# Kernel tuning notes

Measured on AMD Instinct MI355X. Metric: run time of the kernel, lower is better.

The kernel has to match this reference:

```python
import jax, jax.numpy as jnp
import numpy as np

N_NODES = 50000
N_EDGES = 800000
ND = 64   # node_dim
HD = 128  # hidden_dim
ED = 32   # edge_dim


def setup_inputs() -> dict:
    key = jax.random.key(0)
    ks = jax.random.split(key, 16)
    init = lambda k, shape: (jax.random.normal(k, shape, jnp.float32)
                             / np.float32(np.sqrt(shape[0])))
    h = jax.random.normal(ks[0], (N_NODES, ND), jnp.float32)
    x = jax.random.normal(ks[1], (N_NODES, 3), jnp.float32) * 10.0
    edge_index = jax.random.randint(ks[2], (2, N_EDGES), 0, N_NODES, dtype=jnp.int64)
    # realistic edge distances = actual pairwise distances of sampled edges
    edge_dist = jnp.linalg.norm(x[edge_index[0]] - x[edge_index[1]], axis=-1)
    in_dim = 2 * ND + ED
    return {
        "h": h, "x": x, "edge_index": edge_index, "edge_dist": edge_dist,
        # edge_mlp: Linear(1, ED) -> SiLU -> Linear(ED, ED)
        "We1": init(ks[3], (1, ED)), "be1": jnp.zeros((ED,), jnp.float32),
        "We2": init(ks[4], (ED, ED)), "be2": jnp.zeros((ED,), jnp.float32),
        # node_mlp: Linear(in_dim, HD) -> SiLU -> Linear(HD, ND)
        "Wn1": init(ks[5], (in_dim, HD)), "bn1": jnp.zeros((HD,), jnp.float32),
        "Wn2": init(ks[6], (HD, ND)), "bn2": jnp.zeros((ND,), jnp.float32),
        # coord_mlp: Linear(in_dim, HD) -> SiLU -> Linear(HD, 1, bias=False)
        "Wc1": init(ks[7], (in_dim, HD)), "bc1": jnp.zeros((HD,), jnp.float32),
        "Wc2": init(ks[8], (HD, 1)),
    }


def reference(h, x, edge_index, edge_dist,
              We1, be1, We2, be2,
              Wn1, bn1, Wn2, bn2,
              Wc1, bc1, Wc2):
    n = h.shape[0]
    src, dst = edge_index[0], edge_index[1]
    # edge_mlp on scalar distance -> [E, ED]
    e = jax.nn.silu(edge_dist[:, None] @ We1 + be1) @ We2 + be2
    # gather + concat -> [E, 2*ND + ED]
    m_input = jnp.concatenate([h[src], h[dst], e], axis=-1)
    # node messages [E, ND]
    m = jax.nn.silu(m_input @ Wn1 + bn1) @ Wn2 + bn2
    h_agg = jax.ops.segment_sum(m, dst, num_segments=n)
    # coord update weight [E, 1]
    coord_weight = jax.nn.silu(m_input @ Wc1 + bc1) @ Wc2
    dir_vec = x[src] - x[dst]
    dir_len = jnp.clip(jnp.linalg.norm(dir_vec, axis=-1, keepdims=True), 1e-8)
    coord_update = coord_weight * (dir_vec / dir_len)
    x_agg = jax.ops.segment_sum(coord_update, dst, num_segments=n)
    return h + h_agg, x + x_agg
```

## Files before the change

kernel.cpp:

```cpp
#include <hip/hip_runtime.h>


#define NN 50000
#define NE 800000
#define NDIM 64
#define HDIM 128
#define EDIM 32
#define NTILES (NE / 64)
#define MSTRIDE 168
#define HSTRIDE 136
#define NH (NN * NDIM)
#define NX (NN * 3)

typedef __bf16 bf16x8 __attribute__((ext_vector_type(8)));
typedef float f32x4 __attribute__((ext_vector_type(4)));
typedef unsigned short ushort8 __attribute__((ext_vector_type(8)));
typedef unsigned short ushort4v __attribute__((ext_vector_type(4)));

__device__ __forceinline__ unsigned short f2bf(float f) {
    union { float f; unsigned int u; } c; c.f = f;
    unsigned int r = c.u + 0x7fffu + ((c.u >> 16) & 1u);
    return (unsigned short)(r >> 16);
}
__device__ __forceinline__ float bf2f(unsigned short u) {
    union { unsigned int u; float f; } c; c.u = ((unsigned int)u) << 16;
    return c.f;
}
__device__ __forceinline__ float silu(float v) { return v / (1.0f + __expf(-v)); }

__device__ __forceinline__ bf16x8 ld_frag(const unsigned short* p) {
    union { ushort8 u; bf16x8 v; } c;
    c.u = *(const ushort8*)p;
    return c.v;
}
__device__ __forceinline__ bf16x8 mk_frag(const unsigned short* u) {
    union { ushort8 uu; bf16x8 v; } c;
#pragma unroll
    for (int j = 0; j < 8; ++j) c.uu[j] = u[j];
    return c.v;
}

__global__ void init_out(const float* __restrict__ h, const float* __restrict__ x,
                         float* __restrict__ out) {
    int i = blockIdx.x * 256 + threadIdx.x;
    if (i < NH) out[i] = h[i];
    else if (i < NH + NX) out[i] = x[i - NH];
}

__global__ __launch_bounds__(256, 2) void egnn_edges(
    const float* __restrict__ h, const float* __restrict__ x,
    const int* __restrict__ srcg, const int* __restrict__ dstg,
    const float* __restrict__ dist,
    const float* __restrict__ We1, const float* __restrict__ be1,
    const float* __restrict__ We2, const float* __restrict__ be2,
    const float* __restrict__ Wn1, const float* __restrict__ bn1,
    const float* __restrict__ Wn2, const float* __restrict__ bn2,
    const float* __restrict__ Wc1, const float* __restrict__ bc1,
    const float* __restrict__ Wc2,
    float* __restrict__ outh, float* __restrict__ outx) {

    __shared__ __align__(16) unsigned short mlds[64 * MSTRIDE];
    __shared__ __align__(16) unsigned short hl[64 * HSTRIDE];
    __shared__ int src_l[64];
    __shared__ int dst_l[64];
    __shared__ float dist_l[64];
    __shared__ float we1_l[32], be1_l[32], be2_l[32];
    __shared__ float we2_l[32 * 32];
    __shared__ float wc2_l[128];
    __shared__ float part_l[256];

    const int tid  = threadIdx.x;
    const int w    = tid >> 6;
    const int lane = tid & 63;
    const int l15  = lane & 15;
    const int quad = lane >> 4;

    if (tid < 32) { we1_l[tid] = We1[tid]; be1_l[tid] = be1[tid]; be2_l[tid] = be2[tid]; }
    if (tid < 128) wc2_l[tid] = Wc2[tid];
    for (int i = tid; i < 1024; i += 256) we2_l[i] = We2[i];

    bf16x8 wn1f[5][2], wc1f[5][2];
#pragma unroll
    for (int kc = 0; kc < 5; ++kc) {
#pragma unroll
        for (int nt = 0; nt < 2; ++nt) {
            unsigned short un[8], uc[8];
            const int n = w * 32 + nt * 16 + l15;
#pragma unroll
            for (int j = 0; j < 8; ++j) {
                const int k = kc * 32 + quad * 8 + j;
                un[j] = f2bf(Wn1[k * HDIM + n]);
                uc[j] = f2bf(Wc1[k * HDIM + n]);
            }
            wn1f[kc][nt] = mk_frag(un);
            wc1f[kc][nt] = mk_frag(uc);
        }
    }
    bf16x8 wn2f[4];
#pragma unroll
    for (int kc = 0; kc < 4; ++kc) {
        unsigned short u[8];
        const int n = w * 16 + l15;
#pragma unroll
        for (int j = 0; j < 8; ++j) {
            const int k = kc * 32 + quad * 8 + j;
            u[j] = f2bf(Wn2[k * NDIM + n]);
        }
        wn2f[kc] = mk_frag(u);
    }
    const float biasN0 = bn1[w * 32 + l15];
    const float biasN1 = bn1[w * 32 + 16 + l15];
    const float biasC0 = bc1[w * 32 + l15];
    const float biasC1 = bc1[w * 32 + 16 + l15];
    const float bias2v = bn2[w * 16 + l15];

    for (int tile = blockIdx.x; tile < NTILES; tile += gridDim.x) {
        __syncthreads();

        if (tid < 64) {
            const int e = tile * 64 + tid;
            src_l[tid] = srcg[e];
            dst_l[tid] = dstg[e];
            dist_l[tid] = dist[e];
        }
        __syncthreads();

        {
            const int c4 = tid & 15, sub = tid >> 4;
#pragma unroll
            for (int it = 0; it < 4; ++it) {
                const int el = sub + it * 16;
                const float4 hs = *(const float4*)(h + (size_t)src_l[el] * NDIM + c4 * 4);
                const float4 hd = *(const float4*)(h + (size_t)dst_l[el] * NDIM + c4 * 4);
                ushort4v us = { f2bf(hs.x), f2bf(hs.y), f2bf(hs.z), f2bf(hs.w) };
                ushort4v ud = { f2bf(hd.x), f2bf(hd.y), f2bf(hd.z), f2bf(hd.w) };
                *(ushort4v*)&mlds[el * MSTRIDE + c4 * 4] = us;
                *(ushort4v*)&mlds[el * MSTRIDE + 64 + c4 * 4] = ud;
            }
        }
        {
            const int el = tid >> 2, part = tid & 3;
            const float dv = dist_l[el];
            float o[8];
#pragma unroll
            for (int j = 0; j < 8; ++j) o[j] = be2_l[part * 8 + j];
#pragma unroll
            for (int k = 0; k < 32; ++k) {
                const float sk = silu(dv * we1_l[k] + be1_l[k]);
#pragma unroll
                for (int j = 0; j < 8; ++j) o[j] += sk * we2_l[k * 32 + part * 8 + j];
            }
            ushort4v a = { f2bf(o[0]), f2bf(o[1]), f2bf(o[2]), f2bf(o[3]) };
            ushort4v b = { f2bf(o[4]), f2bf(o[5]), f2bf(o[6]), f2bf(o[7]) };
            *(ushort4v*)&mlds[el * MSTRIDE + 128 + part * 8] = a;
            *(ushort4v*)&mlds[el * MSTRIDE + 128 + part * 8 + 4] = b;
        }
        __syncthreads();

        f32x4 accN[4][2], accC[4][2];
#pragma unroll
        for (int mt = 0; mt < 4; ++mt) {
            accN[mt][0] = (f32x4){biasN0, biasN0, biasN0, biasN0};
            accN[mt][1] = (f32x4){biasN1, biasN1, biasN1, biasN1};
            accC[mt][0] = (f32x4){biasC0, biasC0, biasC0, biasC0};
            accC[mt][1] = (f32x4){biasC1, biasC1, biasC1, biasC1};
        }
#pragma unroll
        for (int kc = 0; kc < 5; ++kc) {
            bf16x8 af[4];
#pragma unroll
            for (int mt = 0; mt < 4; ++mt)
                af[mt] = ld_frag(&mlds[(mt * 16 + l15) * MSTRIDE + kc * 32 + quad * 8]);
#pragma unroll
            for (int mt = 0; mt < 4; ++mt) {
#pragma unroll
                for (int nt = 0; nt < 2; ++nt) {
                    accN[mt][nt] = __builtin_amdgcn_mfma_f32_16x16x32_bf16(
                        af[mt], wn1f[kc][nt], accN[mt][nt], 0, 0, 0);
                    accC[mt][nt] = __builtin_amdgcn_mfma_f32_16x16x32_bf16(
                        af[mt], wc1f[kc][nt], accC[mt][nt], 0, 0, 0);
                }
            }
        }

#pragma unroll
        for (int mt = 0; mt < 4; ++mt)
#pragma unroll
            for (int nt = 0; nt < 2; ++nt)
#pragma unroll
                for (int r = 0; r < 4; ++r)
                    hl[(mt * 16 + quad * 4 + r) * HSTRIDE + w * 32 + nt * 16 + l15] =
                        f2bf(silu(accN[mt][nt][r]));
        __syncthreads();

        f32x4 acc2[4];
#pragma unroll
        for (int mt = 0; mt < 4; ++mt) acc2[mt] = (f32x4){bias2v, bias2v, bias2v, bias2v};
#pragma unroll
        for (int kc = 0; kc < 4; ++kc) {
#pragma unroll
            for (int mt = 0; mt < 4; ++mt) {
                bf16x8 a2 = ld_frag(&hl[(mt * 16 + l15) * HSTRIDE + kc * 32 + quad * 8]);
                acc2[mt] = __builtin_amdgcn_mfma_f32_16x16x32_bf16(a2, wn2f[kc], acc2[mt], 0, 0, 0);
            }
        }
#pragma unroll
        for (int mt = 0; mt < 4; ++mt) {
#pragma unroll
            for (int r = 0; r < 4; ++r) {
                const int el = mt * 16 + quad * 4 + r;
                atomicAdd(outh + (size_t)dst_l[el] * NDIM + w * 16 + l15, acc2[mt][r]);
            }
        }
        __syncthreads();

#pragma unroll
        for (int mt = 0; mt < 4; ++mt)
#pragma unroll
            for (int nt = 0; nt < 2; ++nt)
#pragma unroll
                for (int r = 0; r < 4; ++r)
                    hl[(mt * 16 + quad * 4 + r) * HSTRIDE + w * 32 + nt * 16 + l15] =
                        f2bf(silu(accC[mt][nt][r]));
        __syncthreads();

        {
            const int el = tid & 63, part = tid >> 6;
            float s = 0.0f;
#pragma unroll
            for (int k = 0; k < 32; ++k) {
                const int kk = part * 32 + k;
                s += bf2f(hl[el * HSTRIDE + kk]) * wc2_l[kk];
            }
            part_l[part * 64 + el] = s;
        }
        __syncthreads();

        if (tid < 64) {
            const float cw = part_l[tid] + part_l[64 + tid] + part_l[128 + tid] + part_l[192 + tid];
            const int sn = src_l[tid], dn = dst_l[tid];
            const float dx = x[sn * 3 + 0] - x[dn * 3 + 0];
            const float dy = x[sn * 3 + 1] - x[dn * 3 + 1];
            const float dz = x[sn * 3 + 2] - x[dn * 3 + 2];
            float len = sqrtf(dx * dx + dy * dy + dz * dz);
            len = fmaxf(len, 1e-8f);
            const float f = cw / len;
            atomicAdd(outx + (size_t)dn * 3 + 0, f * dx);
            atomicAdd(outx + (size_t)dn * 3 + 1, f * dy);
            atomicAdd(outx + (size_t)dn * 3 + 2, f * dz);
        }
    }
}

extern "C" void kernel_launch(void* const* d_in, const int* in_sizes, int n_in,
                              void* d_out, int out_size, void* d_ws, size_t ws_size,
                              hipStream_t stream) {
    const float* h    = (const float*)d_in[0];
    const float* x    = (const float*)d_in[1];
    const int*   ei   = (const int*)d_in[2];
    const float* dist = (const float*)d_in[3];
    const float* We1  = (const float*)d_in[4];
    const float* be1  = (const float*)d_in[5];
    const float* We2  = (const float*)d_in[6];
    const float* be2  = (const float*)d_in[7];
    const float* Wn1  = (const float*)d_in[8];
    const float* bn1  = (const float*)d_in[9];
    const float* Wn2  = (const float*)d_in[10];
    const float* bn2  = (const float*)d_in[11];
    const float* Wc1  = (const float*)d_in[12];
    const float* bc1  = (const float*)d_in[13];
    const float* Wc2  = (const float*)d_in[14];

    float* outh = (float*)d_out;
    float* outx = outh + (size_t)NH;

    init_out<<<(NH + NX + 255) / 256, 256, 0, stream>>>(h, x, (float*)d_out);
    egnn_edges<<<512, 256, 0, stream>>>(h, x, ei, ei + NE, dist,
                                        We1, be1, We2, be2,
                                        Wn1, bn1, Wn2, bn2,
                                        Wc1, bc1, Wc2,
                                        outh, outx);
}
```

Measured before the change: 415.3 us.

## Fold edge-MLP second layer into Wn1/Wc1 and reduce coord weights via shuffles

A new prep kernel multiplies We2/be2 into the edge rows of Wn1 and Wc1, so the per-edge 32x32 edge-MLP matmul is dropped and only the SiLU of the first layer is written into the message tile. The coord-MLP output projection is now computed in registers from the MFMA accumulators, using a butterfly shuffle reduction, which removes one LDS write pass, one LDS read pass and two barriers per tile. It also switches to native bf16 conversion and fast division. Rounding changes slightly because the folded weights are cast to bf16 and the edge features take a different path.

New measurement: 446.3 us. 1.07x slower.

```diff
diff --git a/kernel.cpp b/kernel.cpp
--- a/kernel.cpp
+++ b/kernel.cpp
@@ -12,21 +12,24 @@
 #define NH (NN * NDIM)
 #define NX (NN * 3)
 
+#define WS_WN1P 0
+#define WS_WC1P 20480
+#define WS_BN1P 40960
+#define WS_BC1P 41088
+
 typedef __bf16 bf16x8 __attribute__((ext_vector_type(8)));
 typedef float f32x4 __attribute__((ext_vector_type(4)));
 typedef unsigned short ushort8 __attribute__((ext_vector_type(8)));
 typedef unsigned short ushort4v __attribute__((ext_vector_type(4)));
 
 __device__ __forceinline__ unsigned short f2bf(float f) {
-    union { float f; unsigned int u; } c; c.f = f;
-    unsigned int r = c.u + 0x7fffu + ((c.u >> 16) & 1u);
-    return (unsigned short)(r >> 16);
-}
-__device__ __forceinline__ float bf2f(unsigned short u) {
-    union { unsigned int u; float f; } c; c.u = ((unsigned int)u) << 16;
-    return c.f;
-}
-__device__ __forceinline__ float silu(float v) { return v / (1.0f + __expf(-v)); }
+    union { __bf16 b; unsigned short u; } c;
+    c.b = (__bf16)f;
+    return c.u;
+}
+__device__ __forceinline__ float silu(float v) {
+    return __fdividef(v, 1.0f + __expf(-v));
+}
 
 __device__ __forceinline__ bf16x8 ld_frag(const unsigned short* p) {
     union { ushort8 u; bf16x8 v; } c;
@@ -47,26 +50,56 @@
     else if (i < NH + NX) out[i] = x[i - NH];
 }
 
+__global__ __launch_bounds__(128) void fold_weights(
+    const float* __restrict__ We2, const float* __restrict__ be2,
+    const float* __restrict__ Wn1, const float* __restrict__ bn1,
+    const float* __restrict__ Wc1, const float* __restrict__ bc1,
+    float* __restrict__ ws) {
+    const int b = blockIdx.x;
+    const int col = threadIdx.x;
+    if (b < 320) {
+        const int path = (b >= 160);
+        const float* W = path ? Wc1 : Wn1;
+        float* Wp = ws + (path ? WS_WC1P : WS_WN1P);
+        const int r = path ? (b - 160) : b;
+        if (r < 128) {
+            Wp[r * 128 + col] = W[r * 128 + col];
+        } else {
+            const int j = r - 128;
+            float s = 0.0f;
+#pragma unroll
+            for (int n = 0; n < 32; ++n)
+                s += We2[j * 32 + n] * W[(128 + n) * 128 + col];
+            Wp[r * 128 + col] = s;
+        }
+    } else {
+        const int path = b - 320;
+        const float* W = path ? Wc1 : Wn1;
+        const float* bb = path ? bc1 : bn1;
+        float* bp = ws + (path ? WS_BC1P : WS_BN1P);
+        float s = bb[col];
+#pragma unroll
+        for (int n = 0; n < 32; ++n)
+            s += be2[n] * W[(128 + n) * 128 + col];
+        bp[col] = s;
+    }
+}
+
 __global__ __launch_bounds__(256, 2) void egnn_edges(
     const float* __restrict__ h, const float* __restrict__ x,
     const int* __restrict__ srcg, const int* __restrict__ dstg,
     const float* __restrict__ dist,
     const float* __restrict__ We1, const float* __restrict__ be1,
-    const float* __restrict__ We2, const float* __restrict__ be2,
-    const float* __restrict__ Wn1, const float* __restrict__ bn1,
     const float* __restrict__ Wn2, const float* __restrict__ bn2,
-    const float* __restrict__ Wc1, const float* __restrict__ bc1,
     const float* __restrict__ Wc2,
+    const float* __restrict__ wsW,
     float* __restrict__ outh, float* __restrict__ outx) {
 
     __shared__ __align__(16) unsigned short mlds[64 * MSTRIDE];
     __shared__ __align__(16) unsigned short hl[64 * HSTRIDE];
     __shared__ int src_l[64];
     __shared__ int dst_l[64];
-    __shared__ float dist_l[64];
-    __shared__ float we1_l[32], be1_l[32], be2_l[32];
-    __shared__ float we2_l[32 * 32];
-    __shared__ float wc2_l[128];
+    __shared__ float we1_l[32], be1_l[32];
     __shared__ float part_l[256];
 
     const int tid  = threadIdx.x;
@@ -75,9 +108,12 @@
     const int l15  = lane & 15;
     const int quad = lane >> 4;
 
-    if (tid < 32) { we1_l[tid] = We1[tid]; be1_l[tid] = be1[tid]; be2_l[tid] = be2[tid]; }
-    if (tid < 128) wc2_l[tid] = Wc2[tid];
-    for (int i = tid; i < 1024; i += 256) we2_l[i] = We2[i];
+    const float* Wn1p = wsW + WS_WN1P;
+    const float* Wc1p = wsW + WS_WC1P;
+    const float* bn1p = wsW + WS_BN1P;
+    const float* bc1p = wsW + WS_BC1P;
+
+    if (tid < 32) { we1_l[tid] = We1[tid]; be1_l[tid] = be1[tid]; }
 
     bf16x8 wn1f[5][2], wc1f[5][2];
 #pragma unroll
@@ -89,8 +125,8 @@
 #pragma unroll
             for (int j = 0; j < 8; ++j) {
                 const int k = kc * 32 + quad * 8 + j;
-                un[j] = f2bf(Wn1[k * HDIM + n]);
-                uc[j] = f2bf(Wc1[k * HDIM + n]);
+                un[j] = f2bf(Wn1p[k * HDIM + n]);
+                uc[j] = f2bf(Wc1p[k * HDIM + n]);
             }
             wn1f[kc][nt] = mk_frag(un);
             wc1f[kc][nt] = mk_frag(uc);
@@ -108,11 +144,13 @@
         }
         wn2f[kc] = mk_frag(u);
     }
-    const float biasN0 = bn1[w * 32 + l15];
-    const float biasN1 = bn1[w * 32 + 16 + l15];
-    const float biasC0 = bc1[w * 32 + l15];
-    const float biasC1 = bc1[w * 32 + 16 + l15];
+    const float biasN0 = bn1p[w * 32 + l15];
+    const float biasN1 = bn1p[w * 32 + 16 + l15];
+    const float biasC0 = bc1p[w * 32 + l15];
+    const float biasC1 = bc1p[w * 32 + 16 + l15];
     const float bias2v = bn2[w * 16 + l15];
+    const float wcA = Wc2[w * 32 + l15];
+    const float wcB = Wc2[w * 32 + 16 + l15];
 
     for (int tile = blockIdx.x; tile < NTILES; tile += gridDim.x) {
         __syncthreads();
@@ -121,7 +159,6 @@
             const int e = tile * 64 + tid;
             src_l[tid] = srcg[e];
             dst_l[tid] = dstg[e];
-            dist_l[tid] = dist[e];
         }
         __syncthreads();
 
@@ -139,21 +176,13 @@
             }
         }
         {
-            const int el = tid >> 2, part = tid & 3;
-            const float dv = dist_l[el];
-            float o[8];
-#pragma unroll
-            for (int j = 0; j < 8; ++j) o[j] = be2_l[part * 8 + j];
-#pragma unroll
-            for (int k = 0; k < 32; ++k) {
-                const float sk = silu(dv * we1_l[k] + be1_l[k]);
-#pragma unroll
-                for (int j = 0; j < 8; ++j) o[j] += sk * we2_l[k * 32 + part * 8 + j];
-            }
-            ushort4v a = { f2bf(o[0]), f2bf(o[1]), f2bf(o[2]), f2bf(o[3]) };
-            ushort4v b = { f2bf(o[4]), f2bf(o[5]), f2bf(o[6]), f2bf(o[7]) };
-            *(ushort4v*)&mlds[el * MSTRIDE + 128 + part * 8] = a;
-            *(ushort4v*)&mlds[el * MSTRIDE + 128 + part * 8 + 4] = b;
+            const int el = tid >> 2, j0 = (tid & 3) * 8;
+            const float dv = dist[tile * 64 + el];
+            ushort8 u;
+#pragma unroll
+            for (int j = 0; j < 8; ++j)
+                u[j] = f2bf(silu(dv * we1_l[j0 + j] + be1_l[j0 + j]));
+            *(ushort8*)&mlds[el * MSTRIDE + 128 + j0] = u;
         }
         __syncthreads();
 
@@ -191,6 +220,44 @@
                 for (int r = 0; r < 4; ++r)
                     hl[(mt * 16 + quad * 4 + r) * HSTRIDE + w * 32 + nt * 16 + l15] =
                         f2bf(silu(accN[mt][nt][r]));
+
+        {
+            float p[16];
+#pragma unroll
+            for (int mt = 0; mt < 4; ++mt)
+#pragma unroll
+                for (int r = 0; r < 4; ++r)
+                    p[mt * 4 + r] = silu(accC[mt][0][r]) * wcA + silu(accC[mt][1][r]) * wcB;
+
+            float q8[8];
+#pragma unroll
+            for (int i = 0; i < 8; ++i) {
+                const float send = (l15 & 8) ? p[i] : p[i + 8];
+                const float recv = __shfl_xor(send, 8, 64);
+                q8[i] = ((l15 & 8) ? p[i + 8] : p[i]) + recv;
+            }
+            float q4[4];
+#pragma unroll
+            for (int i = 0; i < 4; ++i) {
+                const float send = (l15 & 4) ? q8[i] : q8[i + 4];
+                const float recv = __shfl_xor(send, 4, 64);
+                q4[i] = ((l15 & 4) ? q8[i + 4] : q8[i]) + recv;
+            }
+            float q2[2];
+#pragma unroll
+            for (int i = 0; i < 2; ++i) {
+                const float send = (l15 & 2) ? q4[i] : q4[i + 2];
+                const float recv = __shfl_xor(send, 2, 64);
+                q2[i] = ((l15 & 2) ? q4[i + 2] : q4[i]) + recv;
+            }
+            {
+                const float send = (l15 & 1) ? q2[0] : q2[1];
+                const float recv = __shfl_xor(send, 1, 64);
+                const float tot = ((l15 & 1) ? q2[1] : q2[0]) + recv;
+                const int edge = (l15 >> 2) * 16 + quad * 4 + (l15 & 3);
+                part_l[w * 64 + edge] = tot;
+            }
+        }
         __syncthreads();
 
         f32x4 acc2[4];
@@ -212,29 +279,6 @@
                 atomicAdd(outh + (size_t)dst_l[el] * NDIM + w * 16 + l15, acc2[mt][r]);
             }
         }
-        __syncthreads();
-
-#pragma unroll
-        for (int mt = 0; mt < 4; ++mt)
-#pragma unroll
-            for (int nt = 0; nt < 2; ++nt)
-#pragma unroll
-                for (int r = 0; r < 4; ++r)
-                    hl[(mt * 16 + quad * 4 + r) * HSTRIDE + w * 32 + nt * 16 + l15] =
-                        f2bf(silu(accC[mt][nt][r]));
-        __syncthreads();
-
-        {
-            const int el = tid & 63, part = tid >> 6;
-            float s = 0.0f;
-#pragma unroll
-            for (int k = 0; k < 32; ++k) {
-                const int kk = part * 32 + k;
-                s += bf2f(hl[el * HSTRIDE + kk]) * wc2_l[kk];
-            }
-            part_l[part * 64 + el] = s;
-        }
-        __syncthreads();
 
         if (tid < 64) {
             const float cw = part_l[tid] + part_l[64 + tid] + part_l[128 + tid] + part_l[192 + tid];
@@ -273,11 +317,11 @@
 
     float* outh = (float*)d_out;
     float* outx = outh + (size_t)NH;
-
+    float* ws   = (float*)d_ws;
+
+    fold_weights<<<322, 128, 0, stream>>>(We2, be2, Wn1, bn1, Wc1, bc1, ws);
     init_out<<<(NH + NX + 255) / 256, 256, 0, stream>>>(h, x, (float*)d_out);
     egnn_edges<<<512, 256, 0, stream>>>(h, x, ei, ei + NE, dist,
-                                        We1, be1, We2, be2,
-                                        Wn1, bn1, Wn2, bn2,
-                                        Wc1, bc1, Wc2,
+                                        We1, be1, Wn2, bn2, Wc2, ws,
                                         outh, outx);
 }
```
